# Optimization experiments

Measured on AMD Instinct MI355X. Metric: run time of the kernel, lower is better.

## Reference

```python
import jax, jax.numpy as jnp
import numpy as np

N = 100000      # entity nodes
E = 1000000     # edges per relation
D_IN = 256
HID = 128
EPS = 1e-16     # PyG softmax denominator eps
NEG_SLOPE = 0.2 # GATConv default leaky_relu slope


def _gat_conv(x, ei, Ws, Wd, a_s, a_d, b):
    """Single-head GATConv (heads=1, concat=False) with self-loops."""
    n = x.shape[0]
    loop = jnp.arange(n, dtype=ei.dtype)
    src = jnp.concatenate([ei[0], loop])  # [E+N]
    dst = jnp.concatenate([ei[1], loop])
    h_src = x @ Ws                         # [N, HID]
    h_dst = x @ Wd                         # [N, HID]
    a_src = h_src @ a_s                    # [N]
    a_dst = h_dst @ a_d                    # [N]
    e = jax.nn.leaky_relu(a_src[src] + a_dst[dst], NEG_SLOPE)  # [E+N]
    # numerically-stable softmax over incoming edges of each dst node
    m = jax.ops.segment_max(e, dst, num_segments=n)
    ex = jnp.exp(e - m[dst])
    denom = jax.ops.segment_sum(ex, dst, num_segments=n)
    alpha = ex / (denom[dst] + EPS)        # [E+N]
    out = jax.ops.segment_sum(alpha[:, None] * h_src[src], dst, num_segments=n)
    return out + b


def setup_inputs() -> dict:
    key = jax.random.key(0)
    ks = jax.random.split(key, 9)
    s_in = 1.0 / np.sqrt(D_IN)
    s_h = 1.0 / np.sqrt(HID)
    return {
        "x": jax.random.normal(ks[0], (N, D_IN), dtype=jnp.float32),
        "edge_index_r0": jax.random.randint(ks[1], (2, E), 0, N, dtype=jnp.int64)
                         if jax.config.jax_enable_x64 else jax.random.randint(ks[1], (2, E), 0, N).astype(jnp.int32),
        "edge_index_r1": jax.random.randint(ks[2], (2, E), 0, N, dtype=jnp.int64)
                         if jax.config.jax_enable_x64 else jax.random.randint(ks[2], (2, E), 0, N).astype(jnp.int32),
        "W_src": jax.random.normal(ks[3], (2, D_IN, HID), dtype=jnp.float32) * s_in,
        "W_dst": jax.random.normal(ks[4], (2, D_IN, HID), dtype=jnp.float32) * s_in,
        "att_src": jax.random.normal(ks[5], (2, HID), dtype=jnp.float32) * s_h,
        "att_dst": jax.random.normal(ks[6], (2, HID), dtype=jnp.float32) * s_h,
        "bias": jnp.zeros((2, HID), dtype=jnp.float32),
    }


def reference(x, edge_index_r0, edge_index_r1, W_src, W_dst, att_src, att_dst, bias):
    # HeteroConv aggr='sum' over the two entity->entity relations
    out = _gat_conv(x, edge_index_r0, W_src[0], W_dst[0], att_src[0], att_dst[0], bias[0])
    out = out + _gat_conv(x, edge_index_r1, W_src[1], W_dst[1], att_src[1], att_dst[1], bias[1])
    # ELU; dropout p=0.0 is identity
    return jax.nn.elu(out)
```

## Files before the change

### kernel.cpp

```cpp
#include <hip/hip_runtime.h>

typedef __attribute__((ext_vector_type(8))) __bf16 bf16x8;
typedef __attribute__((ext_vector_type(4))) float floatx4;
typedef __attribute__((ext_vector_type(2))) float floatx2;

#define SEG 48

__device__ __forceinline__ float bf2f(unsigned short u) {
    return __uint_as_float(((unsigned)u) << 16);
}
__device__ __forceinline__ unsigned short f2bf(float f) {
    unsigned u = __float_as_uint(f);
    unsigned r = u + 0x7FFFu + ((u >> 16) & 1u);
    return (unsigned short)(r >> 16);
}

__device__ __forceinline__ void canon8(const void* src, unsigned short* dst,
                                       long long idx, int f) {
    if (f) {
        *(uint4*)&dst[idx] = *(const uint4*)((const unsigned short*)src + idx);
    } else {
        const float* sf = (const float*)src;
        unsigned short v[8];
        for (int j = 0; j < 8; ++j) v[j] = f2bf(sf[idx + j]);
        *(uint4*)&dst[idx] = *(const uint4*)v;
    }
}

__global__ __launch_bounds__(256) void detect2_k(
    const unsigned short* __restrict__ xs,
    const void* __restrict__ Ws, const void* __restrict__ Wd,
    const void* __restrict__ as, const void* __restrict__ ad,
    const void* __restrict__ b,
    int* __restrict__ flag, float* __restrict__ vecs,
    unsigned short* __restrict__ bsb) {
    __shared__ int sred[256];
    __shared__ int sflag;
    int tid = threadIdx.x;
    int cnt = 0;
    for (int j = 0; j < 16; ++j) {
        unsigned short u = xs[(tid * 16 + j) * 2];
        int e = (u >> 7) & 0xFF;
        cnt += (e >= 96 && e <= 159) ? 1 : 0;
    }
    sred[tid] = cnt;
    __syncthreads();
    for (int s = 128; s > 0; s >>= 1) {
        if (tid < s) sred[tid] += sred[tid + s];
        __syncthreads();
    }
    if (tid == 0) { sflag = (sred[0] > 2048) ? 1 : 0; *flag = sflag; }
    __syncthreads();
    int f = sflag;
    int k = tid;
    for (int r = 0; r < 2; ++r) {
        float s = 0.f, t = 0.f;
        if (f) {
            const uint4* wsr = (const uint4*)((const unsigned short*)Ws + (size_t)r * 32768 + (size_t)k * 128);
            const uint4* wdr = (const uint4*)((const unsigned short*)Wd + (size_t)r * 32768 + (size_t)k * 128);
            const uint4* av  = (const uint4*)((const unsigned short*)as + r * 128);
            const uint4* dv  = (const uint4*)((const unsigned short*)ad + r * 128);
#pragma unroll 4
            for (int i = 0; i < 16; ++i) {
                uint4 w4 = wsr[i], a4 = av[i], v4 = wdr[i], d4 = dv[i];
                const unsigned* wu = (const unsigned*)&w4;
                const unsigned* au = (const unsigned*)&a4;
                const unsigned* vu = (const unsigned*)&v4;
                const unsigned* du = (const unsigned*)&d4;
#pragma unroll
                for (int j = 0; j < 4; ++j) {
                    s += bf2f((unsigned short)(wu[j] & 0xFFFFu)) * bf2f((unsigned short)(au[j] & 0xFFFFu));
                    s += bf2f((unsigned short)(wu[j] >> 16))     * bf2f((unsigned short)(au[j] >> 16));
                    t += bf2f((unsigned short)(vu[j] & 0xFFFFu)) * bf2f((unsigned short)(du[j] & 0xFFFFu));
                    t += bf2f((unsigned short)(vu[j] >> 16))     * bf2f((unsigned short)(du[j] >> 16));
                }
            }
        } else {
            const float4* wsr = (const float4*)((const float*)Ws + (size_t)r * 32768 + (size_t)k * 128);
            const float4* wdr = (const float4*)((const float*)Wd + (size_t)r * 32768 + (size_t)k * 128);
            const float4* av  = (const float4*)((const float*)as + r * 128);
            const float4* dv  = (const float4*)((const float*)ad + r * 128);
#pragma unroll 4
            for (int i = 0; i < 32; ++i) {
                float4 w4 = wsr[i], a4 = av[i], v4 = wdr[i], d4 = dv[i];
                s += w4.x * a4.x + w4.y * a4.y + w4.z * a4.z + w4.w * a4.w;
                t += v4.x * d4.x + v4.y * d4.y + v4.z * d4.z + v4.w * d4.w;
            }
        }
        vecs[(r * 2 + 0) * 256 + k] = s;
        vecs[(r * 2 + 1) * 256 + k] = t;
    }
    if (tid < 32) canon8(b, bsb, (long long)tid * 8, f);
}

__global__ __launch_bounds__(256) void pre_k(
    const void* __restrict__ xraw, unsigned short* __restrict__ xb,
    const float* __restrict__ vecs, float* __restrict__ aout, int n, int canB,
    const void* __restrict__ Ws, unsigned short* __restrict__ Bt,
    const int* __restrict__ flag) {
    __shared__ float sv[1024];
    int b = blockIdx.x, tid = threadIdx.x;
    if (b < canB) {
        for (int j = 0; j < 4; ++j) sv[j * 256 + tid] = vecs[j * 256 + tid];
        __syncthreads();
        int lane = tid & 63, wave = tid >> 6;
        int f = *flag;
        for (int rr = 0; rr < 8; ++rr) {
            int row = b * 32 + wave * 8 + rr;
            if (row >= n) break;
            float xf[4];
            if (f) {
                uint2 u = *(const uint2*)((const unsigned short*)xraw + (size_t)row * 256 + lane * 4);
                xf[0] = bf2f((unsigned short)(u.x & 0xFFFF));
                xf[1] = bf2f((unsigned short)(u.x >> 16));
                xf[2] = bf2f((unsigned short)(u.y & 0xFFFF));
                xf[3] = bf2f((unsigned short)(u.y >> 16));
            } else {
                float4 fv = *(const float4*)((const float*)xraw + (size_t)row * 256 + lane * 4);
                xf[0] = fv.x; xf[1] = fv.y; xf[2] = fv.z; xf[3] = fv.w;
                unsigned short v[4] = {f2bf(fv.x), f2bf(fv.y), f2bf(fv.z), f2bf(fv.w)};
                *(uint2*)&xb[(size_t)row * 256 + lane * 4] = *(const uint2*)v;
            }
            float s[4] = {0.f, 0.f, 0.f, 0.f};
            for (int j = 0; j < 4; ++j)
                for (int q = 0; q < 4; ++q)
                    s[j] += xf[q] * sv[j * 256 + lane * 4 + q];
            for (int j = 0; j < 4; ++j)
                for (int off = 32; off > 0; off >>= 1)
                    s[j] += __shfl_down(s[j], off);
            if (lane == 0)
                for (int j = 0; j < 4; ++j) aout[(size_t)j * n + row] = s[j];
        }
        return;
    }
    b -= canB;
    if (b < 256) {
        int i = b * 256 + tid;
        int f = *flag;
        int r = i >> 15, rem = i & 32767;
        int k = rem >> 7, nn = rem & 127;
        unsigned short w = f ? ((const unsigned short*)Ws)[i]
                             : f2bf(((const float*)Ws)[i]);
        Bt[(size_t)r * 32768 + nn * 256 + k] = w;
    }
}

__device__ __forceinline__ void gload_lds16(const void* g, void* l) {
    __builtin_amdgcn_global_load_lds((const __attribute__((address_space(1))) void*)g,
                                     (__attribute__((address_space(3))) void*)l, 16, 0, 0);
}

__global__ __launch_bounds__(256) void histgemm_k(
    const int* __restrict__ ei0, const int* __restrict__ ei1,
    const float* __restrict__ avals, int* __restrict__ cnt,
    unsigned long long* __restrict__ pair0, unsigned long long* __restrict__ pair1,
    int E_, int n, int histB, int period,
    const void* __restrict__ x_raw, const unsigned short* __restrict__ xb,
    const unsigned short* __restrict__ Btg, unsigned short* __restrict__ hout,
    int gemmB, const int* __restrict__ flag) {
    __shared__ __align__(16) unsigned short As[128 * 64];
    __shared__ __align__(16) unsigned short Bs[128 * 64];
    int b = blockIdx.x, tid = threadIdx.x;
    int bq = b / period;
    if (b - bq * period == 0) {
        if (bq >= gemmB) return;
        const unsigned short* x = (*flag) ? (const unsigned short*)x_raw : xb;
        const int r = bq & 1;
        const unsigned short* bt = Btg + (size_t)r * 32768;
        unsigned short* h = hout + (size_t)r * n * 128;
        const int r0 = (bq >> 1) * 128;
        int lane = tid & 63, wave = tid >> 6;
        int wm = wave >> 1, wn = wave & 1;
        floatx4 acc[4][4];
        for (int mt = 0; mt < 4; ++mt)
            for (int nt = 0; nt < 4; ++nt)
                acc[mt][nt] = (floatx4){0.f, 0.f, 0.f, 0.f};
        int srow = lane >> 3, q = lane & 7;
        int m16 = lane & 15, qb = lane >> 4;
        for (int k0 = 0; k0 < 256; k0 += 64) {
            for (int i = 0; i < 4; ++i) {
                int L = wave * 4 + i;
                int row = L * 8 + srow;
                int sw = ((q ^ (row & 7)) << 3);
                int grow = min(r0 + row, n - 1);
                gload_lds16(x + (size_t)grow * 256 + k0 + sw, &As[L * 512]);
                gload_lds16(bt + (size_t)row * 256 + k0 + sw, &Bs[L * 512]);
            }
            __syncthreads();
            for (int s = 0; s < 2; ++s) {
                int qr = qb + s * 4;
                bf16x8 af[4], bfv[4];
                for (int mt = 0; mt < 4; ++mt) {
                    int row = wm * 64 + mt * 16 + m16;
                    af[mt] = *(const bf16x8*)&As[row * 64 + ((qr ^ (row & 7)) << 3)];
                }
                for (int nt = 0; nt < 4; ++nt) {
                    int row = wn * 64 + nt * 16 + m16;
                    bfv[nt] = *(const bf16x8*)&Bs[row * 64 + ((qr ^ (row & 7)) << 3)];
                }
                for (int mt = 0; mt < 4; ++mt)
                    for (int nt = 0; nt < 4; ++nt)
                        acc[mt][nt] = __builtin_amdgcn_mfma_f32_16x16x32_bf16(
                            af[mt], bfv[nt], acc[mt][nt], 0, 0, 0);
            }
            __syncthreads();
        }
        for (int mt = 0; mt < 4; ++mt) {
            int baser = r0 + wm * 64 + mt * 16 + qb * 4;
            for (int nt = 0; nt < 4; ++nt) {
                int c = wn * 64 + nt * 16 + m16;
                for (int i = 0; i < 4; ++i) {
                    int gr = baser + i;
                    if (gr < n) h[(size_t)gr * 128 + c] = f2bf(acc[mt][nt][i]);
                }
            }
        }
        return;
    }
    int oid = b - bq - 1;
    if (oid >= histB) return;
    int rel = oid & 1;
    int t = (oid >> 1) * 256 + tid;
    if (t >= E_ + n) return;
    const int* ei = rel ? ei1 : ei0;
    const float* as_ = avals + (rel ? 2 * (size_t)n : 0);
    const float* ad_ = avals + (rel ? 3 * (size_t)n : (size_t)n);
    unsigned long long* pair = rel ? pair1 : pair0;
    int* c = cnt + (rel ? n : 0);
    int s, d;
    if (t < E_) { s = ei[t]; d = ei[E_ + t]; } else { s = t - E_; d = s; }
    float e = as_[s] + ad_[d];
    e = e > 0.f ? e : 0.2f * e;
    float w = __expf(e);
    int pos;
    if (t < E_) {
        int rank = atomicAdd(&c[d], 1);
        rank = min(rank, SEG - 2);
        pos = d * SEG + 1 + rank;
    } else {
        pos = d * SEG;
    }
    pair[pos] = ((unsigned long long)__float_as_uint(w) << 32) | (unsigned)s;
}

__device__ __forceinline__ void acc8pk(floatx2* a, float w, const uint4& hv) {
    floatx2 wv = {w, w};
    const unsigned u[4] = {hv.x, hv.y, hv.z, hv.w};
#pragma unroll
    for (int k = 0; k < 4; ++k) {
        floatx2 hf;
        hf.x = __uint_as_float(u[k] << 16);
        hf.y = __uint_as_float(u[k] & 0xFFFF0000u);
        asm("v_pk_fma_f32 %0, %1, %2, %0" : "+v"(a[k]) : "v"(wv), "v"(hf));
    }
}

__global__ __launch_bounds__(256) void agg_k(
    const int* __restrict__ cnt,
    const unsigned long long* __restrict__ pair0,
    const unsigned long long* __restrict__ pair1,
    const char* __restrict__ h0, const char* __restrict__ h1,
    const unsigned short* __restrict__ bias, void* __restrict__ out,
    int n, const int* __restrict__ flag) {
    int wave = threadIdx.x >> 6, lane = threadIdx.x & 63;
    int g = lane >> 4, l = lane & 15;
    unsigned l4 = (unsigned)l << 4;
    int d = blockIdx.x * 4 + wave;
    if (d >= n) return;

    int validA = min(cnt[d] + 1, SEG);
    int validB = min(cnt[n + d] + 1, SEG);
    int nIt = (max(validA, validB) + 7) >> 3;
    int i = d * SEG + g;
    int s0 = g, s1 = g + 4;
    unsigned nm1 = (unsigned)(n - 1);

    float denA = 0.f, denB = 0.f;
    floatx2 aA[4], aB[4];
#pragma unroll
    for (int k = 0; k < 4; ++k) {
        aA[k] = (floatx2){0.f, 0.f};
        aB[k] = (floatx2){0.f, 0.f};
    }

    unsigned long long pA0 = pair0[i];
    unsigned long long pA1 = pair0[i + 4];
    unsigned long long pB0 = pair1[i];
    unsigned long long pB1 = pair1[i + 4];

    for (int it = 0; it < nIt; ++it) {
        unsigned xA0 = min((unsigned)pA0, nm1);
        unsigned xA1 = min((unsigned)pA1, nm1);
        unsigned xB0 = min((unsigned)pB0, nm1);
        unsigned xB1 = min((unsigned)pB1, nm1);
        uint4 hA0 = *(const uint4*)(h0 + ((xA0 << 8) + l4));
        uint4 hA1 = *(const uint4*)(h0 + ((xA1 << 8) + l4));
        uint4 hB0 = *(const uint4*)(h1 + ((xB0 << 8) + l4));
        uint4 hB1 = *(const uint4*)(h1 + ((xB1 << 8) + l4));
        float wA0 = (s0 < validA) ? __uint_as_float((unsigned)(pA0 >> 32)) : 0.f;
        float wA1 = (s1 < validA) ? __uint_as_float((unsigned)(pA1 >> 32)) : 0.f;
        float wB0 = (s0 < validB) ? __uint_as_float((unsigned)(pB0 >> 32)) : 0.f;
        float wB1 = (s1 < validB) ? __uint_as_float((unsigned)(pB1 >> 32)) : 0.f;
        i += 8; s0 += 8; s1 += 8;
        pA0 = pair0[i];
        pA1 = pair0[i + 4];
        pB0 = pair1[i];
        pB1 = pair1[i + 4];
        denA += wA0 + wA1;
        denB += wB0 + wB1;
        acc8pk(aA, wA0, hA0);
        acc8pk(aA, wA1, hA1);
        acc8pk(aB, wB0, hB0);
        acc8pk(aB, wB1, hB1);
    }

    denA += __shfl_xor(denA, 16);
    denA += __shfl_xor(denA, 32);
    denB += __shfl_xor(denB, 16);
    denB += __shfl_xor(denB, 32);
    float invA = __builtin_amdgcn_rcpf(denA + 1e-16f);
    float invB = __builtin_amdgcn_rcpf(denB + 1e-16f);
    floatx2 ivA = {invA, invA}, ivB = {invB, invB};
#pragma unroll
    for (int k = 0; k < 4; ++k) {
        asm("v_pk_mul_f32 %0, %0, %1" : "+v"(aA[k]) : "v"(ivA));
        asm("v_pk_fma_f32 %0, %1, %2, %0" : "+v"(aA[k]) : "v"(aB[k]), "v"(ivB));
    }
    float t8[8] = {aA[0].x, aA[0].y, aA[1].x, aA[1].y,
                   aA[2].x, aA[2].y, aA[3].x, aA[3].y};

    uint4 b0 = *(const uint4*)&bias[l * 8];
    uint4 b1 = *(const uint4*)&bias[128 + l * 8];
    const unsigned* b0u = (const unsigned*)&b0;
    const unsigned* b1u = (const unsigned*)&b1;
    float v[8];
#pragma unroll
    for (int j = 0; j < 8; ++j) {
        float s = t8[j];
        s += __shfl_xor(s, 16);
        s += __shfl_xor(s, 32);
        unsigned w0 = b0u[j >> 1], w1 = b1u[j >> 1];
        float bb = bf2f((unsigned short)((j & 1) ? (w0 >> 16) : (w0 & 0xFFFFu)))
                 + bf2f((unsigned short)((j & 1) ? (w1 >> 16) : (w1 & 0xFFFFu)));
        float t = s + bb;
        v[j] = t > 0.f ? t : (__expf(t) - 1.f);
    }
    if (g == 0) {
        if (*flag) {
            unsigned pk[4];
            for (int j = 0; j < 4; ++j)
                pk[j] = ((unsigned)f2bf(v[2 * j + 1]) << 16) | (unsigned)f2bf(v[2 * j]);
            ((uint4*)out)[(size_t)d * 16 + l] = *(const uint4*)pk;
        } else {
            float4 f0 = make_float4(v[0], v[1], v[2], v[3]);
            float4 f1 = make_float4(v[4], v[5], v[6], v[7]);
            ((float4*)out)[(size_t)d * 32 + l * 2] = f0;
            ((float4*)out)[(size_t)d * 32 + l * 2 + 1] = f1;
        }
    }
}

static inline char* carve(char*& p, size_t bytes) {
    char* r = p;
    p += (bytes + 255) & ~(size_t)255;
    return r;
}

extern "C" void kernel_launch(void* const* d_in, const int* in_sizes, int n_in,
                              void* d_out, int out_size, void* d_ws, size_t ws_size,
                              hipStream_t stream) {
    (void)n_in; (void)out_size; (void)ws_size;
    const void* x_raw  = d_in[0];
    const int*  ei0    = (const int*)d_in[1];
    const int*  ei1    = (const int*)d_in[2];
    const void* Ws_raw = d_in[3];
    const void* Wd_raw = d_in[4];
    const void* as_raw = d_in[5];
    const void* ad_raw = d_in[6];
    const void* b_raw  = d_in[7];

    const int n = in_sizes[0] / 256;
    const int e = in_sizes[1] / 2;
    const int tot = e + n;

    char* p = (char*)d_ws;
    float* avals = (float*)carve(p, (size_t)4 * n * 4);
    int*   cnt   = (int*)carve(p, (size_t)2 * n * 4);
    float* vecs  = (float*)carve(p, 1024 * 4);
    int*   flag  = (int*)carve(p, 256);
    unsigned short* xb = (unsigned short*)carve(p, (size_t)(n + 128) * 256 * 2);
    unsigned long long* pair0 = (unsigned long long*)carve(p, ((size_t)n * SEG + 64) * 8);
    unsigned long long* pair1 = (unsigned long long*)carve(p, ((size_t)n * SEG + 64) * 8);
    unsigned short* h0  = (unsigned short*)carve(p, (size_t)2 * n * 128 * 2);
    unsigned short* h1  = h0 + (size_t)n * 128;
    unsigned short* Bt  = (unsigned short*)carve(p, 65536 * 2);
    unsigned short* bsb = (unsigned short*)carve(p, 256 * 2);

    hipMemsetAsync(cnt, 0, (size_t)2 * n * 4, stream);

    detect2_k<<<1, 256, 0, stream>>>((const unsigned short*)x_raw, Ws_raw, Wd_raw,
                                     as_raw, ad_raw, b_raw, flag, vecs, bsb);

    int canB = (n + 31) / 32;
    pre_k<<<canB + 256, 256, 0, stream>>>(x_raw, xb, vecs, avals, n, canB,
                                          Ws_raw, Bt, flag);

    int gbT = (tot + 255) / 256;
    int histB = gbT * 2;
    int gemmB = ((n + 127) / 128) * 2;
    int period = (histB + gemmB - 1) / gemmB + 1;
    int G = gemmB * period;
    histgemm_k<<<G, 256, 0, stream>>>(
        ei0, ei1, avals, cnt, pair0, pair1, e, n, histB, period,
        x_raw, xb, Bt, h0, gemmB, flag);

    agg_k<<<(n + 3) / 4, 256, 0, stream>>>(cnt, pair0, pair1,
                                           (const char*)h0, (const char*)h1,
                                           bsb, d_out, n, flag);
}
```

Measured before the change: 447.2 us.

## Drop LDS staging in GEMM tiles and fold count zeroing into pre-kernel

The GEMM portion of the fused hist/GEMM kernel now uses 64-row tiles and loads A and B fragments straight from global memory into MFMA operands, with no LDS staging or barriers. This frees LDS so more hist blocks can co-reside, and doubles the number of GEMM blocks. The separate memset of the count array is replaced by extra blocks in the pre-kernel that zero it, removing one launch. In exchange, each wave re-reads the weight matrix from global/L2, and the uncoalesced 16-byte loads may raise memory traffic.

```diff
diff --git a/kernel.cpp b/kernel.cpp
--- a/kernel.cpp
+++ b/kernel.cpp
@@ -97,6 +97,7 @@
     const void* __restrict__ xraw, unsigned short* __restrict__ xb,
     const float* __restrict__ vecs, float* __restrict__ aout, int n, int canB,
     const void* __restrict__ Ws, unsigned short* __restrict__ Bt,
+    int* __restrict__ cnt, int zcB,
     const int* __restrict__ flag) {
     __shared__ float sv[1024];
     int b = blockIdx.x, tid = threadIdx.x;
@@ -142,12 +143,13 @@
         unsigned short w = f ? ((const unsigned short*)Ws)[i]
                              : f2bf(((const float*)Ws)[i]);
         Bt[(size_t)r * 32768 + nn * 256 + k] = w;
-    }
-}
-
-__device__ __forceinline__ void gload_lds16(const void* g, void* l) {
-    __builtin_amdgcn_global_load_lds((const __attribute__((address_space(1))) void*)g,
-                                     (__attribute__((address_space(3))) void*)l, 16, 0, 0);
+        return;
+    }
+    b -= 256;
+    if (b < zcB) {
+        int idx = b * 256 + tid;
+        if (idx * 4 < 2 * n) ((uint4*)cnt)[idx] = make_uint4(0u, 0u, 0u, 0u);
+    }
 }
 
 __global__ __launch_bounds__(256) void histgemm_k(
@@ -158,8 +160,6 @@
     const void* __restrict__ x_raw, const unsigned short* __restrict__ xb,
     const unsigned short* __restrict__ Btg, unsigned short* __restrict__ hout,
     int gemmB, const int* __restrict__ flag) {
-    __shared__ __align__(16) unsigned short As[128 * 64];
-    __shared__ __align__(16) unsigned short Bs[128 * 64];
     int b = blockIdx.x, tid = threadIdx.x;
     int bq = b / period;
     if (b - bq * period == 0) {
@@ -168,53 +168,31 @@
         const int r = bq & 1;
         const unsigned short* bt = Btg + (size_t)r * 32768;
         unsigned short* h = hout + (size_t)r * n * 128;
-        const int r0 = (bq >> 1) * 128;
+        const int r0 = (bq >> 1) * 64;
         int lane = tid & 63, wave = tid >> 6;
-        int wm = wave >> 1, wn = wave & 1;
-        floatx4 acc[4][4];
-        for (int mt = 0; mt < 4; ++mt)
-            for (int nt = 0; nt < 4; ++nt)
-                acc[mt][nt] = (floatx4){0.f, 0.f, 0.f, 0.f};
-        int srow = lane >> 3, q = lane & 7;
         int m16 = lane & 15, qb = lane >> 4;
-        for (int k0 = 0; k0 < 256; k0 += 64) {
-            for (int i = 0; i < 4; ++i) {
-                int L = wave * 4 + i;
-                int row = L * 8 + srow;
-                int sw = ((q ^ (row & 7)) << 3);
-                int grow = min(r0 + row, n - 1);
-                gload_lds16(x + (size_t)grow * 256 + k0 + sw, &As[L * 512]);
-                gload_lds16(bt + (size_t)row * 256 + k0 + sw, &Bs[L * 512]);
-            }
-            __syncthreads();
-            for (int s = 0; s < 2; ++s) {
-                int qr = qb + s * 4;
-                bf16x8 af[4], bfv[4];
-                for (int mt = 0; mt < 4; ++mt) {
-                    int row = wm * 64 + mt * 16 + m16;
-                    af[mt] = *(const bf16x8*)&As[row * 64 + ((qr ^ (row & 7)) << 3)];
-                }
-                for (int nt = 0; nt < 4; ++nt) {
-                    int row = wn * 64 + nt * 16 + m16;
-                    bfv[nt] = *(const bf16x8*)&Bs[row * 64 + ((qr ^ (row & 7)) << 3)];
-                }
-                for (int mt = 0; mt < 4; ++mt)
-                    for (int nt = 0; nt < 4; ++nt)
-                        acc[mt][nt] = __builtin_amdgcn_mfma_f32_16x16x32_bf16(
-                            af[mt], bfv[nt], acc[mt][nt], 0, 0, 0);
-            }
-            __syncthreads();
+        int rowg = min(r0 + wave * 16 + m16, n - 1);
+        const unsigned short* arow = x + (size_t)rowg * 256 + qb * 8;
+        const unsigned short* brow = bt + (size_t)m16 * 256 + qb * 8;
+        floatx4 acc[8];
+#pragma unroll
+        for (int c = 0; c < 8; ++c) acc[c] = (floatx4){0.f, 0.f, 0.f, 0.f};
+#pragma unroll
+        for (int ks = 0; ks < 8; ++ks) {
+            bf16x8 a = *(const bf16x8*)(arow + ks * 32);
+#pragma unroll
+            for (int c = 0; c < 8; ++c) {
+                bf16x8 bb = *(const bf16x8*)(brow + (size_t)c * 16 * 256 + ks * 32);
+                acc[c] = __builtin_amdgcn_mfma_f32_16x16x32_bf16(a, bb, acc[c], 0, 0, 0);
+            }
         }
-        for (int mt = 0; mt < 4; ++mt) {
-            int baser = r0 + wm * 64 + mt * 16 + qb * 4;
-            for (int nt = 0; nt < 4; ++nt) {
-                int c = wn * 64 + nt * 16 + m16;
-                for (int i = 0; i < 4; ++i) {
-                    int gr = baser + i;
-                    if (gr < n) h[(size_t)gr * 128 + c] = f2bf(acc[mt][nt][i]);
-                }
-            }
-        }
+        int baser = r0 + wave * 16 + qb * 4;
+#pragma unroll
+        for (int c = 0; c < 8; ++c)
+            for (int i2 = 0; i2 < 4; ++i2) {
+                int gr = baser + i2;
+                if (gr < n) h[(size_t)gr * 128 + c * 16 + m16] = f2bf(acc[c][i2]);
+            }
         return;
     }
     int oid = b - bq - 1;
@@ -396,18 +374,17 @@
     unsigned short* Bt  = (unsigned short*)carve(p, 65536 * 2);
     unsigned short* bsb = (unsigned short*)carve(p, 256 * 2);
 
-    hipMemsetAsync(cnt, 0, (size_t)2 * n * 4, stream);
-
     detect2_k<<<1, 256, 0, stream>>>((const unsigned short*)x_raw, Ws_raw, Wd_raw,
                                      as_raw, ad_raw, b_raw, flag, vecs, bsb);
 
     int canB = (n + 31) / 32;
-    pre_k<<<canB + 256, 256, 0, stream>>>(x_raw, xb, vecs, avals, n, canB,
-                                          Ws_raw, Bt, flag);
+    int zcB = (2 * n / 4 + 255) / 256;
+    pre_k<<<canB + 256 + zcB, 256, 0, stream>>>(x_raw, xb, vecs, avals, n, canB,
+                                                Ws_raw, Bt, cnt, zcB, flag);
 
     int gbT = (tot + 255) / 256;
     int histB = gbT * 2;
-    int gemmB = ((n + 127) / 128) * 2;
+    int gemmB = ((n + 63) / 64) * 2;
     int period = (histB + gemmB - 1) / gemmB + 1;
     int G = gemmB * period;
     histgemm_k<<<G, 256, 0, stream>>>(
```

New measurement: 697.0 us. +55.9%, slower.
